# Performance work log

Hardware: AMD Instinct MI355X
Metric: run time of the kernel (lower is better)

Reference implementation:

```python
import jax, jax.numpy as jnp
import numpy as np

B, C_IN, C_OUT, H, K = 256, 64, 128, 1039, 6  # batch, in_ch, out_ch, num_hexagons, max_neighbors


def _make_neighbors(rng, num_hex, max_n):
    # valid neighbor indices first, -1 padding at the end (matches torch init)
    nb = np.full((num_hex, max_n), -1, dtype=np.int64)
    counts = rng.integers(3, max_n + 1, size=num_hex)
    for i in range(num_hex):
        nb[i, :counts[i]] = rng.choice(num_hex, size=counts[i], replace=False)
    return nb


def setup_inputs() -> dict:
    key = jax.random.key(0)
    k1, k2, k3 = jax.random.split(key, 3)
    rng = np.random.default_rng(0)
    x = jax.random.normal(k1, (B, C_IN, H), dtype=jnp.float32)
    neighbors = jnp.asarray(_make_neighbors(rng, H, K))
    weight_center = jax.random.normal(k2, (C_OUT, C_IN), dtype=jnp.float32) / np.sqrt(C_IN)
    weight_neighbors = jax.random.normal(k3, (C_OUT, C_IN, K), dtype=jnp.float32) / np.sqrt(C_IN * K)
    bias = jnp.zeros((C_OUT,), dtype=jnp.float32)
    return {"x": x, "neighbors": neighbors, "weight_center": weight_center,
            "weight_neighbors": weight_neighbors, "bias": bias}


def reference(x, neighbors, weight_center, weight_neighbors, bias):
    # x: [B, C_in, H]; neighbors: [H, K] with -1 padding at the tail
    mask = (neighbors >= 0)                        # [H, K]
    safe_idx = jnp.where(mask, neighbors, 0)       # [H, K]
    # gather neighbor features and zero out padded slots: [B, C_in, H, K]
    neigh = x[:, :, safe_idx] * mask.astype(x.dtype)[None, None, :, :]
    center = jnp.einsum('bch,oc->boh', x, weight_center)
    neigh_contrib = jnp.einsum('bchk,ock->boh', neigh, weight_neighbors)
    total_valid = (mask.sum(axis=-1) + 1).astype(x.dtype)  # [H]
    out = (center + neigh_contrib) / total_valid[None, None, :] + bias[None, :, None]
    return out
```

## Files before the change

### kernel.cpp

```cpp
#include <hip/hip_runtime.h>

#define BATCH 256
#define CIN   64
#define COUT  128
#define HEX   1039
#define KNB   6
#define KDIM  448
#define BN    64
#define NTH   17
#define CPX   544
#define THT   32
#define NTT   33
#define TBLK  (BATCH * NTT)
#define HROWS (HEX + 1)

typedef __attribute__((ext_vector_type(8))) short bf16x8;
typedef __attribute__((ext_vector_type(4))) float f32x4;

__device__ __forceinline__ unsigned short f2bf(float f) {
    unsigned int u = __builtin_bit_cast(unsigned int, f);
    u += 0x7fffu + ((u >> 16) & 1);
    return (unsigned short)(u >> 16);
}

__global__ __launch_bounds__(256) void k_pre(const float* __restrict__ x,
                                             const float* __restrict__ wc,
                                             const float* __restrict__ wn,
                                             const int* __restrict__ nb,
                                             unsigned short* __restrict__ xt,
                                             unsigned short* __restrict__ wf,
                                             float* __restrict__ invtv,
                                             int* __restrict__ gidx) {
    int bid = blockIdx.x;
    int tid = threadIdx.x;
    if (bid < TBLK) {
        int b  = bid / NTT;
        int ht = bid % NTT;
        int h  = ht * THT + (tid >> 3);
        int c8 = (tid & 7) * 8;
        if (h >= HEX) return;
        const float* xb = x + (size_t)b * (CIN * HEX) + h;
        bf16x8 v;
        #pragma unroll
        for (int k = 0; k < 8; ++k)
            v[k] = (short)f2bf(xb[(size_t)(c8 + k) * HEX]);
        *(bf16x8*)(xt + (size_t)b * (HROWS * CIN) + (size_t)h * CIN + c8) = v;
        return;
    }
    int blk = bid - TBLK;
    if (blk < 224) {
        int e    = blk * 256 + tid;
        int j    = e & 7;
        int lane = (e >> 3) & 63;
        int mt   = (e >> 9) & 7;
        int kb   = e >> 12;
        int o  = mt * 16 + (lane & 15);
        int kd = kb * 32 + (lane >> 4) * 8 + j;
        int jn = kd >> 6;
        int c  = kd & 63;
        float v = (jn == 0) ? wc[o * CIN + c]
                            : wn[(o * CIN + c) * KNB + (jn - 1)];
        wf[e] = f2bf(v);
    } else if (blk < 229) {
        int h = (blk - 224) * 256 + tid;
        if (h < HEX) {
            int cnt = 1;
            #pragma unroll
            for (int k = 0; k < KNB; ++k) cnt += (nb[h * KNB + k] >= 0) ? 1 : 0;
            invtv[h] = 1.0f / (float)cnt;
        }
    } else if (blk < 259) {
        int e = (blk - 229) * 256 + tid;
        if (e < NTH * KDIM) {
            int ht = e / KDIM;
            int p  = e - ht * KDIM;
            int jn = p >> 6;
            int n  = p & 63;
            int h  = ht * 64 + n;
            int g  = HEX;
            if (h < HEX) {
                if (jn == 0) g = h;
                else {
                    int t = nb[h * KNB + (jn - 1)];
                    if (t >= 0) g = t;
                }
            }
            gidx[e] = g;
        }
    } else {
        int b = tid;
        bf16x8 z = {};
        unsigned short* row = xt + (size_t)b * (HROWS * CIN) + (size_t)HEX * CIN;
        #pragma unroll
        for (int k = 0; k < 8; ++k)
            *(bf16x8*)(row + k * 8) = z;
    }
}

__global__ __launch_bounds__(512, 4) void k_gemm(const unsigned short* __restrict__ xt,
                                                 const unsigned short* __restrict__ wf,
                                                 const int* __restrict__ gidx,
                                                 const float* __restrict__ invtv,
                                                 const float* __restrict__ bias,
                                                 float* __restrict__ out) {
    __shared__ __align__(16) unsigned short Bs[KDIM * CIN];

    int bid = blockIdx.x;
    int id2 = (bid & 7) * CPX + (bid >> 3);
    int b   = id2 / NTH;
    int ht  = id2 - b * NTH;
    int h0  = ht * BN;
    int tid = threadIdx.x;
    int lane = tid & 63;
    int wv   = tid >> 6;

    {
        const unsigned short* xtb = xt + (size_t)b * (HROWS * CIN);
        const int* gt = gidx + ht * KDIM;
        int r8 = lane >> 3;
        int cc = lane & 7;
        int gs[7];
        #pragma unroll
        for (int i = 0; i < 7; ++i)
            gs[i] = gt[(wv * 7 + i) * 8 + r8];
        #pragma unroll
        for (int i = 0; i < 7; ++i) {
            int t = wv * 7 + i;
            bf16x8 v = *(const bf16x8*)(xtb + (size_t)gs[i] * CIN + (cc << 3));
            *(bf16x8*)(Bs + t * 512 + r8 * 64 + ((cc ^ r8) << 3)) = v;
        }
    }
    __syncthreads();

    int quad = lane >> 4;
    int l16  = lane & 15;
    int m    = wv & 3;
    int nh   = wv >> 2;
    int swz  = l16 & 7;

    f32x4 acc[2][2] = {};

    const bf16x8* wfv = (const bf16x8*)wf;
    const char*   BsB = (const char*)Bs;

    bf16x8 a0[2], a1[2], a2[2];
    #pragma unroll
    for (int mi = 0; mi < 2; ++mi) {
        a0[mi] = wfv[(0 * 8 + 2 * m + mi) * 64 + lane];
        a1[mi] = wfv[(1 * 8 + 2 * m + mi) * 64 + lane];
    }

    #pragma unroll
    for (int ks = 0; ks < 14; ++ks) {
        if (ks < 12) {
            #pragma unroll
            for (int mi = 0; mi < 2; ++mi)
                a2[mi] = wfv[((ks + 2) * 8 + 2 * m + mi) * 64 + lane];
        }
        int jn    = ks >> 1;
        int chunk = (((ks & 1) << 2) + quad) ^ swz;
        #pragma unroll
        for (int nt = 0; nt < 2; ++nt) {
            int n = nh * 32 + nt * 16 + l16;
            bf16x8 bb = *(const bf16x8*)(BsB + (((jn << 6) + n) << 7) + (chunk << 4));
            acc[0][nt] = __builtin_amdgcn_mfma_f32_16x16x32_bf16(a0[0], bb, acc[0][nt], 0, 0, 0);
            acc[1][nt] = __builtin_amdgcn_mfma_f32_16x16x32_bf16(a0[1], bb, acc[1][nt], 0, 0, 0);
        }
        a0[0] = a1[0]; a0[1] = a1[1];
        a1[0] = a2[0]; a1[1] = a2[1];
    }

    float* outb = out + (size_t)b * ((size_t)COUT * HEX);
    #pragma unroll
    for (int nt = 0; nt < 2; ++nt) {
        int h = h0 + nh * 32 + nt * 16 + l16;
        if (h >= HEX) continue;
        float s = invtv[h];
        #pragma unroll
        for (int mi = 0; mi < 2; ++mi) {
            #pragma unroll
            for (int r = 0; r < 4; ++r) {
                int o = (2 * m + mi) * 16 + quad * 4 + r;
                outb[(size_t)o * HEX + h] = acc[mi][nt][r] * s + bias[o];
            }
        }
    }
}

extern "C" void kernel_launch(void* const* d_in, const int* in_sizes, int n_in,
                              void* d_out, int out_size, void* d_ws, size_t ws_size,
                              hipStream_t stream) {
    const float* x    = (const float*)d_in[0];
    const int*   nb   = (const int*)d_in[1];
    const float* wc   = (const float*)d_in[2];
    const float* wn   = (const float*)d_in[3];
    const float* bias = (const float*)d_in[4];
    float*       out  = (float*)d_out;

    const size_t INVTV_OFF = (size_t)KDIM * COUT * 2;
    const size_t GIDX_OFF  = 131072;
    const size_t XT_OFF    = 196608;
    unsigned short* wf    = (unsigned short*)d_ws;
    float*          invtv = (float*)((char*)d_ws + INVTV_OFF);
    int*            gidx  = (int*)((char*)d_ws + GIDX_OFF);
    unsigned short* xt    = (unsigned short*)((char*)d_ws + XT_OFF);

    hipLaunchKernelGGL(k_pre,  dim3(TBLK + 260), dim3(256), 0, stream,
                       x, wc, wn, nb, xt, wf, invtv, gidx);
    hipLaunchKernelGGL(k_gemm, dim3(BATCH * NTH), dim3(512), 0, stream,
                       xt, wf, gidx, invtv, bias, out);
}
```

Baseline: 240.1 us.

## Fuse transpose into GEMM with per-batch LDS-resident activations and in-kernel gather

Replaces the global bf16 transposed copy of x and the precomputed gather index table with one block per batch that transposes the whole [H,C] slab into swizzled LDS (about 133KB) and then loops over all hex tiles. Neighbor indices and valid counts are computed in-kernel, and all weight fragments are held in registers across tiles. This removes the intermediate global round-trip and the extra prep work. The cost is a grid of only 256 blocks with low occupancy, and a large register footprint for the A fragments.

```diff
diff --git a/kernel.cpp b/kernel.cpp
--- a/kernel.cpp
+++ b/kernel.cpp
@@ -5,14 +5,9 @@
 #define COUT  128
 #define HEX   1039
 #define KNB   6
-#define KDIM  448
-#define BN    64
+#define ZROW  HEX
 #define NTH   17
-#define CPX   544
-#define THT   32
-#define NTT   33
-#define TBLK  (BATCH * NTT)
-#define HROWS (HEX + 1)
+#define LDSB  ((HEX + 1) * 128)
 
 typedef __attribute__((ext_vector_type(8))) short bf16x8;
 typedef __attribute__((ext_vector_type(4))) float f32x4;
@@ -23,166 +18,139 @@
     return (unsigned short)(u >> 16);
 }
 
-__global__ __launch_bounds__(256) void k_pre(const float* __restrict__ x,
-                                             const float* __restrict__ wc,
-                                             const float* __restrict__ wn,
-                                             const int* __restrict__ nb,
-                                             unsigned short* __restrict__ xt,
-                                             unsigned short* __restrict__ wf,
-                                             float* __restrict__ invtv,
-                                             int* __restrict__ gidx) {
-    int bid = blockIdx.x;
-    int tid = threadIdx.x;
-    if (bid < TBLK) {
-        int b  = bid / NTT;
-        int ht = bid % NTT;
-        int h  = ht * THT + (tid >> 3);
-        int c8 = (tid & 7) * 8;
-        if (h >= HEX) return;
-        const float* xb = x + (size_t)b * (CIN * HEX) + h;
-        bf16x8 v;
+__global__ __launch_bounds__(256) void k_prep(const float* __restrict__ wc,
+                                              const float* __restrict__ wn,
+                                              unsigned short* __restrict__ wf) {
+    int e    = blockIdx.x * 256 + threadIdx.x;
+    int j    = e & 7;
+    int lane = (e >> 3) & 63;
+    int mt   = (e >> 9) & 7;
+    int kb   = e >> 12;
+    int o  = mt * 16 + (lane & 15);
+    int kd = kb * 32 + (lane >> 4) * 8 + j;
+    int jn = kd >> 6;
+    int c  = kd & 63;
+    float v = (jn == 0) ? wc[o * CIN + c]
+                        : wn[(o * CIN + c) * KNB + (jn - 1)];
+    wf[e] = f2bf(v);
+}
+
+__global__ __launch_bounds__(512, 2) void k_main(const float* __restrict__ x,
+                                                 const int* __restrict__ nb,
+                                                 const unsigned short* __restrict__ wf,
+                                                 const float* __restrict__ bias,
+                                                 float* __restrict__ out) {
+    extern __shared__ __align__(16) unsigned short XT[];
+
+    int b    = blockIdx.x;
+    int tid  = threadIdx.x;
+    int lane = tid & 63;
+    int wv   = tid >> 6;
+    int quad = lane >> 4;
+    int l16  = lane & 15;
+    int m    = wv & 3;
+    int nh   = wv >> 2;
+
+    const bf16x8* wfv = (const bf16x8*)wf;
+    bf16x8 A[14][2];
+    #pragma unroll
+    for (int kb = 0; kb < 14; ++kb)
         #pragma unroll
-        for (int k = 0; k < 8; ++k)
-            v[k] = (short)f2bf(xb[(size_t)(c8 + k) * HEX]);
-        *(bf16x8*)(xt + (size_t)b * (HROWS * CIN) + (size_t)h * CIN + c8) = v;
-        return;
-    }
-    int blk = bid - TBLK;
-    if (blk < 224) {
-        int e    = blk * 256 + tid;
-        int j    = e & 7;
-        int lane = (e >> 3) & 63;
-        int mt   = (e >> 9) & 7;
-        int kb   = e >> 12;
-        int o  = mt * 16 + (lane & 15);
-        int kd = kb * 32 + (lane >> 4) * 8 + j;
-        int jn = kd >> 6;
-        int c  = kd & 63;
-        float v = (jn == 0) ? wc[o * CIN + c]
-                            : wn[(o * CIN + c) * KNB + (jn - 1)];
-        wf[e] = f2bf(v);
-    } else if (blk < 229) {
-        int h = (blk - 224) * 256 + tid;
-        if (h < HEX) {
-            int cnt = 1;
+        for (int mi = 0; mi < 2; ++mi)
+            A[kb][mi] = wfv[(kb * 8 + 2 * m + mi) * 64 + lane];
+
+    float bs[2][4];
+    #pragma unroll
+    for (int mi = 0; mi < 2; ++mi)
+        #pragma unroll
+        for (int r = 0; r < 4; ++r)
+            bs[mi][r] = bias[(2 * m + mi) * 16 + quad * 4 + r];
+
+    {
+        const float* xb = x + (size_t)b * (CIN * HEX);
+        for (int t = 0; t < 9; ++t) {
             #pragma unroll
-            for (int k = 0; k < KNB; ++k) cnt += (nb[h * KNB + k] >= 0) ? 1 : 0;
-            invtv[h] = 1.0f / (float)cnt;
-        }
-    } else if (blk < 259) {
-        int e = (blk - 229) * 256 + tid;
-        if (e < NTH * KDIM) {
-            int ht = e / KDIM;
-            int p  = e - ht * KDIM;
-            int jn = p >> 6;
-            int n  = p & 63;
-            int h  = ht * 64 + n;
-            int g  = HEX;
-            if (h < HEX) {
-                if (jn == 0) g = h;
-                else {
-                    int t = nb[h * KNB + (jn - 1)];
-                    if (t >= 0) g = t;
+            for (int u = 0; u < 2; ++u) {
+                int e = t * 1024 + u * 512 + tid;
+                if (e < 8320) {
+                    int h  = e >> 3;
+                    int cc = e & 7;
+                    bf16x8 v = {};
+                    if (h < HEX) {
+                        #pragma unroll
+                        for (int k = 0; k < 8; ++k)
+                            v[k] = (short)f2bf(xb[(size_t)(cc * 8 + k) * HEX + h]);
+                    }
+                    *(bf16x8*)((char*)XT + h * 128 + ((cc ^ (h & 7)) << 4)) = v;
                 }
             }
-            gidx[e] = g;
-        }
-    } else {
-        int b = tid;
-        bf16x8 z = {};
-        unsigned short* row = xt + (size_t)b * (HROWS * CIN) + (size_t)HEX * CIN;
-        #pragma unroll
-        for (int k = 0; k < 8; ++k)
-            *(bf16x8*)(row + k * 8) = z;
-    }
-}
-
-__global__ __launch_bounds__(512, 4) void k_gemm(const unsigned short* __restrict__ xt,
-                                                 const unsigned short* __restrict__ wf,
-                                                 const int* __restrict__ gidx,
-                                                 const float* __restrict__ invtv,
-                                                 const float* __restrict__ bias,
-                                                 float* __restrict__ out) {
-    __shared__ __align__(16) unsigned short Bs[KDIM * CIN];
-
-    int bid = blockIdx.x;
-    int id2 = (bid & 7) * CPX + (bid >> 3);
-    int b   = id2 / NTH;
-    int ht  = id2 - b * NTH;
-    int h0  = ht * BN;
-    int tid = threadIdx.x;
-    int lane = tid & 63;
-    int wv   = tid >> 6;
-
-    {
-        const unsigned short* xtb = xt + (size_t)b * (HROWS * CIN);
-        const int* gt = gidx + ht * KDIM;
-        int r8 = lane >> 3;
-        int cc = lane & 7;
-        int gs[7];
-        #pragma unroll
-        for (int i = 0; i < 7; ++i)
-            gs[i] = gt[(wv * 7 + i) * 8 + r8];
-        #pragma unroll
-        for (int i = 0; i < 7; ++i) {
-            int t = wv * 7 + i;
-            bf16x8 v = *(const bf16x8*)(xtb + (size_t)gs[i] * CIN + (cc << 3));
-            *(bf16x8*)(Bs + t * 512 + r8 * 64 + ((cc ^ r8) << 3)) = v;
         }
     }
     __syncthreads();
 
-    int quad = lane >> 4;
-    int l16  = lane & 15;
-    int m    = wv & 3;
-    int nh   = wv >> 2;
-    int swz  = l16 & 7;
+    int ho = nh * 32 + l16;
+    int rawn[2][6];
+    int voff[2][7];
+    float inv[2];
 
-    f32x4 acc[2][2] = {};
+    auto loadraw = [&](int ht2) {
+        #pragma unroll
+        for (int nt = 0; nt < 2; ++nt) {
+            int h  = ht2 * 64 + ho + nt * 16;
+            int hs = (h < HEX) ? h : 0;
+            #pragma unroll
+            for (int j = 0; j < KNB; ++j)
+                rawn[nt][j] = nb[hs * KNB + j];
+        }
+    };
+    auto offg = [&](int g) { return (g << 7) | ((quad ^ (g & 7)) << 4); };
 
-    const bf16x8* wfv = (const bf16x8*)wf;
-    const char*   BsB = (const char*)Bs;
+    loadraw(0);
+    float* outb = out + (size_t)b * ((size_t)COUT * HEX);
 
-    bf16x8 a0[2], a1[2], a2[2];
-    #pragma unroll
-    for (int mi = 0; mi < 2; ++mi) {
-        a0[mi] = wfv[(0 * 8 + 2 * m + mi) * 64 + lane];
-        a1[mi] = wfv[(1 * 8 + 2 * m + mi) * 64 + lane];
-    }
+    for (int ht = 0; ht < NTH; ++ht) {
+        #pragma unroll
+        for (int nt = 0; nt < 2; ++nt) {
+            int h = ht * 64 + ho + nt * 16;
+            bool hv = (h < HEX);
+            voff[nt][0] = offg(hv ? h : ZROW);
+            int cnt = 1;
+            #pragma unroll
+            for (int j = 0; j < KNB; ++j) {
+                int t2 = rawn[nt][j];
+                bool val = hv && (t2 >= 0);
+                cnt += val ? 1 : 0;
+                voff[nt][j + 1] = offg(val ? t2 : ZROW);
+            }
+            inv[nt] = 1.0f / (float)cnt;
+        }
+        if (ht + 1 < NTH) loadraw(ht + 1);
 
-    #pragma unroll
-    for (int ks = 0; ks < 14; ++ks) {
-        if (ks < 12) {
+        f32x4 acc[2][2] = {};
+        #pragma unroll
+        for (int ks = 0; ks < 14; ++ks) {
+            int jn = ks >> 1;
+            int xr = (ks & 1) << 6;
+            #pragma unroll
+            for (int nt = 0; nt < 2; ++nt) {
+                bf16x8 bb = *(const bf16x8*)((const char*)XT + (voff[nt][jn] ^ xr));
+                acc[0][nt] = __builtin_amdgcn_mfma_f32_16x16x32_bf16(A[ks][0], bb, acc[0][nt], 0, 0, 0);
+                acc[1][nt] = __builtin_amdgcn_mfma_f32_16x16x32_bf16(A[ks][1], bb, acc[1][nt], 0, 0, 0);
+            }
+        }
+
+        #pragma unroll
+        for (int nt = 0; nt < 2; ++nt) {
+            int h = ht * 64 + ho + nt * 16;
+            if (h >= HEX) continue;
+            float s = inv[nt];
             #pragma unroll
             for (int mi = 0; mi < 2; ++mi)
-                a2[mi] = wfv[((ks + 2) * 8 + 2 * m + mi) * 64 + lane];
-        }
-        int jn    = ks >> 1;
-        int chunk = (((ks & 1) << 2) + quad) ^ swz;
-        #pragma unroll
-        for (int nt = 0; nt < 2; ++nt) {
-            int n = nh * 32 + nt * 16 + l16;
-            bf16x8 bb = *(const bf16x8*)(BsB + (((jn << 6) + n) << 7) + (chunk << 4));
-            acc[0][nt] = __builtin_amdgcn_mfma_f32_16x16x32_bf16(a0[0], bb, acc[0][nt], 0, 0, 0);
-            acc[1][nt] = __builtin_amdgcn_mfma_f32_16x16x32_bf16(a0[1], bb, acc[1][nt], 0, 0, 0);
-        }
-        a0[0] = a1[0]; a0[1] = a1[1];
-        a1[0] = a2[0]; a1[1] = a2[1];
-    }
-
-    float* outb = out + (size_t)b * ((size_t)COUT * HEX);
-    #pragma unroll
-    for (int nt = 0; nt < 2; ++nt) {
-        int h = h0 + nh * 32 + nt * 16 + l16;
-        if (h >= HEX) continue;
-        float s = invtv[h];
-        #pragma unroll
-        for (int mi = 0; mi < 2; ++mi) {
-            #pragma unroll
-            for (int r = 0; r < 4; ++r) {
-                int o = (2 * m + mi) * 16 + quad * 4 + r;
-                outb[(size_t)o * HEX + h] = acc[mi][nt][r] * s + bias[o];
-            }
+                #pragma unroll
+                for (int r = 0; r < 4; ++r) {
+                    int o = (2 * m + mi) * 16 + quad * 4 + r;
+                    outb[(size_t)o * HEX + h] = acc[mi][nt][r] * s + bs[mi][r];
+                }
         }
     }
 }
@@ -197,16 +165,16 @@
     const float* bias = (const float*)d_in[4];
     float*       out  = (float*)d_out;
 
-    const size_t INVTV_OFF = (size_t)KDIM * COUT * 2;
-    const size_t GIDX_OFF  = 131072;
-    const size_t XT_OFF    = 196608;
-    unsigned short* wf    = (unsigned short*)d_ws;
-    float*          invtv = (float*)((char*)d_ws + INVTV_OFF);
-    int*            gidx  = (int*)((char*)d_ws + GIDX_OFF);
-    unsigned short* xt    = (unsigned short*)((char*)d_ws + XT_OFF);
+    unsigned short* wf = (unsigned short*)d_ws;
 
-    hipLaunchKernelGGL(k_pre,  dim3(TBLK + 260), dim3(256), 0, stream,
-                       x, wc, wn, nb, xt, wf, invtv, gidx);
-    hipLaunchKernelGGL(k_gemm, dim3(BATCH * NTH), dim3(512), 0, stream,
-                       xt, wf, gidx, invtv, bias, out);
+    static bool s_attr_done = false;
+    if (!s_attr_done) {
+        hipFuncSetAttribute((const void*)k_main,
+                            hipFuncAttributeMaxDynamicSharedMemorySize, LDSB);
+        s_attr_done = true;
+    }
+
+    hipLaunchKernelGGL(k_prep, dim3(224),   dim3(256), 0,    stream, wc, wn, wf);
+    hipLaunchKernelGGL(k_main, dim3(BATCH), dim3(512), LDSB, stream,
+                       x, nb, wf, bias, out);
 }
```

Result: faster. 228.0 us (-5.1%).
